# Kernel tuning notes

Measured on AMD Instinct MI355X. Metric: run time of the kernel, lower is better.

The kernel has to match this reference:

```python
import jax, jax.numpy as jnp
import numpy as np

N = 100000
E = 1600000
NEG_SLOPE = 0.2


def _gat_layer(x, src, dst, W, a_src, a_dst, b, heads, out_ch):
    n = x.shape[0]
    h = (x @ W).reshape(n, heads, out_ch)                      # [N,H,C]
    alpha_src = (h * a_src).sum(-1)                            # [N,H]
    alpha_dst = (h * a_dst).sum(-1)                            # [N,H]
    e = jax.nn.leaky_relu(alpha_src[src] + alpha_dst[dst], NEG_SLOPE)  # [E,H]
    # segment softmax over incoming edges of each destination node
    m = jax.ops.segment_max(e, dst, num_segments=n)            # [N,H]
    ex = jnp.exp(e - m[dst])
    denom = jax.ops.segment_sum(ex, dst, num_segments=n)       # [N,H]
    alpha = ex / (denom[dst] + 1e-16)                          # [E,H]
    msg = h[src] * alpha[:, :, None]                           # [E,H,C]
    out = jax.ops.segment_sum(msg, dst, num_segments=n)        # [N,H,C]
    return out.reshape(n, heads * out_ch) + b


def setup_inputs() -> dict:
    key = jax.random.key(0)
    ks = jax.random.split(key, 10)
    glorot = lambda k, shape: jax.random.normal(k, shape, jnp.float32) * np.sqrt(2.0 / (shape[0] + shape[-1]))
    x = jax.random.normal(ks[0], (N, 5), jnp.float32)
    edge_index = jax.random.randint(ks[1], (2, E), 0, N, jnp.int64)
    return {
        "x": x,
        "edge_index": edge_index,
        "W1": glorot(ks[2], (5, 64)),
        "a_src1": glorot(ks[3], (8, 8)),
        "a_dst1": glorot(ks[4], (8, 8)),
        "b1": jnp.zeros((64,), jnp.float32),
        "W2": glorot(ks[5], (64, 2)),
        "a_src2": glorot(ks[6], (1, 2)),
        "a_dst2": glorot(ks[7], (1, 2)),
        "b2": jnp.zeros((2,), jnp.float32),
    }


def reference(x, edge_index, W1, a_src1, a_dst1, b1, W2, a_src2, a_dst2, b2):
    n = x.shape[0]
    loop = jnp.arange(n, dtype=edge_index.dtype)
    src = jnp.concatenate([edge_index[0], loop])   # PyG GATConv adds self-loops
    dst = jnp.concatenate([edge_index[1], loop])
    # dropout layers are no-ops in eval mode
    h = jax.nn.elu(_gat_layer(x, src, dst, W1, a_src1, a_dst1, b1, heads=8, out_ch=8))
    out = _gat_layer(h, src, dst, W2, a_src2, a_dst2, b2, heads=1, out_ch=2)
    return jax.nn.log_softmax(out, axis=1)
```

## Files before the change

### kernel.cpp

```cpp
#include <hip/hip_runtime.h>
#include <hip/hip_fp16.h>
#include <math.h>
#include <stdint.h>

#define N_NODES 100000
#define N_EDGES 1600000
#define N_TOT   (N_EDGES + N_NODES)
#define NEG_SLOPE 0.2f
#define LOG2E 1.44269504088896340736f

#define CB     128
#define CBBITS 7
#define NCB    ((N_NODES + CB - 1) / CB)
#define TP     2048
#define NPB    ((N_EDGES + TP - 1) / TP)
#define WINB   2560
#define NB_NODE1 ((N_NODES * 8 + 511) / 512)

typedef int nt_int4 __attribute__((ext_vector_type(4)));

__global__ void __launch_bounds__(512) k_np(
        const int* __restrict__ src, const int* __restrict__ dst,
        int* __restrict__ ofsT, unsigned* __restrict__ pairs,
        const float* __restrict__ x, const float* __restrict__ W1,
        const float* __restrict__ a_src1, const float* __restrict__ a_dst1,
        __half* __restrict__ xh, __half* __restrict__ as1h,
        float* __restrict__ ad1) {
    __shared__ int lcnt[1024];
    __shared__ int sm[512];
    __shared__ unsigned stage[TP];
    int t = threadIdx.x;

    if (blockIdx.x >= NPB) {
        int gid  = (blockIdx.x - NPB) * 512 + t;
        int n    = gid >> 3;
        int head = gid & 7;
        if (n >= N_NODES) return;

        float xv[5];
#pragma unroll
        for (int k = 0; k < 5; ++k) xv[k] = x[n * 5 + k];

        float as = 0.f, ad = 0.f;
#pragma unroll
        for (int j = 0; j < 8; ++j) {
            int c = head * 8 + j;
            float acc = 0.f;
#pragma unroll
            for (int k = 0; k < 5; ++k) acc += xv[k] * W1[k * 64 + c];
            as += acc * a_src1[c];
            ad += acc * a_dst1[c];
        }
        as1h[n * 8 + head] = __float2half(as * LOG2E);
        ad1[n * 8 + head] = ad * LOG2E;

        if (head == 0) {
            __half2 p0 = __halves2half2(__float2half(xv[0]), __float2half(xv[1]));
            __half2 p1 = __halves2half2(__float2half(xv[2]), __float2half(xv[3]));
            __half2 p2 = __halves2half2(__float2half(xv[4]), __float2half(0.f));
            __half2 p3 = __halves2half2(__float2half(0.f), __float2half(0.f));
            __half2* xp = (__half2*)&xh[(size_t)n * 8];
            xp[0] = p0; xp[1] = p1; xp[2] = p2; xp[3] = p3;
        }
        return;
    }

    int blk = blockIdx.x;
    int base = blk * TP + t * 4;
    bool act = base < N_EDGES;
    int nE = min(TP, N_EDGES - blk * TP);

    lcnt[t] = 0; lcnt[t + 512] = 0;
    __syncthreads();

    nt_int4 s4, d4;
    if (act) {
        s4 = __builtin_nontemporal_load((const nt_int4*)(src + base));
        d4 = __builtin_nontemporal_load((const nt_int4*)(dst + base));
#pragma unroll
        for (int j = 0; j < 4; ++j) atomicAdd(&lcnt[d4[j] >> CBBITS], 1);
    }
    __syncthreads();

    int b0 = lcnt[t * 2], b1 = lcnt[t * 2 + 1];
    int local = b0 + b1;
    sm[t] = local;
    __syncthreads();
    for (int off = 1; off < 512; off <<= 1) {
        int u = (t >= off) ? sm[t - off] : 0;
        __syncthreads();
        sm[t] += u;
        __syncthreads();
    }
    int run = sm[t] - local;
    lcnt[t * 2] = run; lcnt[t * 2 + 1] = run + b0;
    if (t * 2     <= NCB) ofsT[(size_t)(t * 2)     * NPB + blk] = run;
    if (t * 2 + 1 <= NCB) ofsT[(size_t)(t * 2 + 1) * NPB + blk] = run + b0;
    __syncthreads();

    if (act) {
#pragma unroll
        for (int j = 0; j < 4; ++j) {
            int d = d4[j], s = s4[j];
            int bin = d >> CBBITS;
            int idx = atomicAdd(&lcnt[bin], 1);
            stage[idx] = ((unsigned)(d & (CB - 1)) << 17) | (unsigned)s;
        }
    }
    __syncthreads();
    for (int i = t; i < nE; i += 512)
        pairs[(size_t)blk * TP + i] = stage[i];
}

__global__ void __launch_bounds__(512) k_csr(
        const int* __restrict__ ofsT, const unsigned* __restrict__ pairs,
        int* __restrict__ rbeg, int* __restrict__ rend, int* __restrict__ ssrc) {
    __shared__ unsigned stIn[WINB];
    __shared__ int stOut[WINB];
    __shared__ int lcnt[CB], lofs[CB], lcur[CB];
    __shared__ int wsum[2];
    __shared__ int acur;
    int B = blockIdx.x, t = threadIdx.x;
    int nvalid = min(CB, N_NODES - B * CB);
    int obase = B * WINB;

    if (t < CB) {
        lcnt[t] = (t < nvalid) ? 1 : 0;
        lcur[t] = 1;
    }
    if (t == 0) acur = 0;
    __syncthreads();

    for (int blk = t; blk < NPB; blk += 512) {
        int o0 = ofsT[(size_t)B       * NPB + blk];
        int o1 = ofsT[(size_t)(B + 1) * NPB + blk];
        int n = o1 - o0;
        if (n > 0) {
            int p = atomicAdd(&acur, n);
            const unsigned* pp = pairs + (size_t)blk * TP + o0;
            for (int i = 0; i < n; ++i) {
                unsigned r = pp[i];
                stIn[p + i] = r;
                atomicAdd(&lcnt[r >> 17], 1);
            }
        }
    }
    __syncthreads();
    int m = acur;

    int v = (t < CB) ? lcnt[t] : 0;
    int ln = t & 63, wv = t >> 6;
    int sc = v;
#pragma unroll
    for (int off = 1; off < 64; off <<= 1) {
        int u = __shfl_up(sc, off, 64);
        if (ln >= off) sc += u;
    }
    if (ln == 63 && wv < 2) wsum[wv] = sc;
    __syncthreads();
    int wbase = (wv == 1) ? wsum[0] : 0;
    int ex = wbase + sc - v;
    if (t < CB) {
        lofs[t] = ex;
        int gi = B * CB + t;
        if (gi < N_NODES) {
            rbeg[gi] = obase + ex;
            rend[gi] = obase + ex + v;
            stOut[ex] = gi;
        }
    }
    __syncthreads();

    for (int k = t; k < m; k += 512) {
        unsigned p = stIn[k];
        int dl = p >> 17;
        int idx = atomicAdd(&lcur[dl], 1);
        stOut[lofs[dl] + idx] = (int)(p & 0x1FFFF);
    }
    __syncthreads();

    int tot = m + nvalid;
    for (int i = t; i < tot; i += 512) ssrc[obase + i] = stOut[i];
}

__global__ void __launch_bounds__(256) k_gather1(
        const int* __restrict__ rbeg, const int* __restrict__ rend,
        const int* __restrict__ ssrc, const float4* __restrict__ xh4,
        const __half* __restrict__ as1h, const float* __restrict__ ad1,
        float* __restrict__ xsbuf) {
    int gtid = blockIdx.x * blockDim.x + threadIdx.x;
    int d      = gtid >> 5;
    int lane32 = threadIdx.x & 31;
    if (d >= N_NODES) return;
    int e = lane32 >> 3;
    int h = lane32 & 7;

    int beg = rbeg[d], end = rend[d];
    float adv = ad1[d * 8 + h];
    float c0 = 0.f, c1 = 0.f, c2 = 0.f, c3 = 0.f, c4 = 0.f, den = 0.f;

    for (int k = beg; k < end; k += 8) {
        int kA = k + e, kB = k + 4 + e;
        bool vA = kA < end, vB = kB < end;
        int sA = ssrc[vA ? kA : beg];
        int sB = ssrc[vB ? kB : beg];
        float eA = __half2float(as1h[sA * 8 + h]);
        float eB = __half2float(as1h[sB * 8 + h]);
        float4 xA = xh4[sA];
        float4 xB = xh4[sB];
        float tA = eA + adv; tA = fmaxf(tA, NEG_SLOPE * tA);
        float tB = eB + adv; tB = fmaxf(tB, NEG_SLOPE * tB);
        float wA = vA ? __builtin_amdgcn_exp2f(tA) : 0.f;
        float wB = vB ? __builtin_amdgcn_exp2f(tB) : 0.f;
        float2 A01 = __half22float2(*(__half2*)&xA.x);
        float2 A23 = __half22float2(*(__half2*)&xA.y);
        float2 A4_ = __half22float2(*(__half2*)&xA.z);
        float2 B01 = __half22float2(*(__half2*)&xB.x);
        float2 B23 = __half22float2(*(__half2*)&xB.y);
        float2 B4_ = __half22float2(*(__half2*)&xB.z);
        c0 += wA * A01.x + wB * B01.x;
        c1 += wA * A01.y + wB * B01.y;
        c2 += wA * A23.x + wB * B23.x;
        c3 += wA * A23.y + wB * B23.y;
        c4 += wA * A4_.x + wB * B4_.x;
        den += wA + wB;
    }

#define REDH(x) x += __shfl_xor(x, 8, 64); x += __shfl_xor(x, 16, 64);
    REDH(c0) REDH(c1) REDH(c2) REDH(c3) REDH(c4) REDH(den)
#undef REDH

    if (e == 0) {
        float inv = 1.f / den;
        float* xp = xsbuf + ((size_t)d * 8 + h) * 6;
        *(float2*)(xp + 0) = make_float2(c0 * inv, c1 * inv);
        *(float2*)(xp + 2) = make_float2(c2 * inv, c3 * inv);
        *(float2*)(xp + 4) = make_float2(c4 * inv, 0.f);
    }
}

__global__ void __launch_bounds__(256) k_rec(
        const float* __restrict__ xsbuf, const float* __restrict__ b1,
        const float* __restrict__ W1, const float* __restrict__ W2,
        const float* __restrict__ a_src2, const float* __restrict__ a_dst2,
        float4* __restrict__ rec) {
    int gtid = blockIdx.x * blockDim.x + threadIdx.x;
    int d = gtid >> 3;
    int h = gtid & 7;
    if (d >= N_NODES) return;

    const float* xp = xsbuf + ((size_t)d * 8 + h) * 6;
    float2 p0 = *(const float2*)(xp + 0);
    float2 p1 = *(const float2*)(xp + 2);
    float2 p2 = *(const float2*)(xp + 4);
    float xs[5] = { p0.x, p0.y, p1.x, p1.y, p2.x };

    float4 hA = ((const float4*)b1)[2 * h];
    float4 hB = ((const float4*)b1)[2 * h + 1];
#pragma unroll
    for (int c = 0; c < 5; ++c) {
        float xc = xs[c];
        float4 wA = *(const float4*)(W1 + c * 64 + 8 * h);
        float4 wB = *(const float4*)(W1 + c * 64 + 8 * h + 4);
        hA.x += xc * wA.x; hA.y += xc * wA.y; hA.z += xc * wA.z; hA.w += xc * wA.w;
        hB.x += xc * wB.x; hB.y += xc * wB.y; hB.z += xc * wB.z; hB.w += xc * wB.w;
    }
    float v0 = hA.x, v1 = hA.y, v2 = hA.z, v3 = hA.w;
    float v4 = hB.x, v5 = hB.y, v6 = hB.z, v7 = hB.w;
    v0 = (v0 > 0.f) ? v0 : (__expf(v0) - 1.f);
    v1 = (v1 > 0.f) ? v1 : (__expf(v1) - 1.f);
    v2 = (v2 > 0.f) ? v2 : (__expf(v2) - 1.f);
    v3 = (v3 > 0.f) ? v3 : (__expf(v3) - 1.f);
    v4 = (v4 > 0.f) ? v4 : (__expf(v4) - 1.f);
    v5 = (v5 > 0.f) ? v5 : (__expf(v5) - 1.f);
    v6 = (v6 > 0.f) ? v6 : (__expf(v6) - 1.f);
    v7 = (v7 > 0.f) ? v7 : (__expf(v7) - 1.f);

    const float4* w4 = (const float4*)(W2 + h * 16);
    float4 wq0 = w4[0], wq1 = w4[1], wq2 = w4[2], wq3 = w4[3];
    float h20 = v0 * wq0.x + v1 * wq0.z + v2 * wq1.x + v3 * wq1.z
              + v4 * wq2.x + v5 * wq2.z + v6 * wq3.x + v7 * wq3.z;
    float h21 = v0 * wq0.y + v1 * wq0.w + v2 * wq1.y + v3 * wq1.w
              + v4 * wq2.y + v5 * wq2.w + v6 * wq3.y + v7 * wq3.w;
    h20 += __shfl_xor(h20, 1, 64); h20 += __shfl_xor(h20, 2, 64); h20 += __shfl_xor(h20, 4, 64);
    h21 += __shfl_xor(h21, 1, 64); h21 += __shfl_xor(h21, 2, 64); h21 += __shfl_xor(h21, 4, 64);

    if (h == 0) {
        float as2v = h20 * a_src2[0] + h21 * a_src2[1];
        float ad2v = h20 * a_dst2[0] + h21 * a_dst2[1];
        rec[d] = make_float4(h20, h21, as2v, ad2v);
    }
}

__global__ void k_gather2(const int* __restrict__ rbeg, const int* __restrict__ rend,
                          const int* __restrict__ ssrc, const float4* __restrict__ rec,
                          const float* __restrict__ b2, float* __restrict__ out) {
    int gtid = blockIdx.x * blockDim.x + threadIdx.x;
    int d    = gtid >> 4;
    int lane = gtid & 15;
    if (d >= N_NODES) return;

    int beg = rbeg[d], end = rend[d];
    float adv = rec[d].w;
    float n0 = 0.f, n1 = 0.f, den = 0.f;
    int k = beg + lane;
    for (; k + 16 < end; k += 32) {
        int s0 = ssrc[k], s1 = ssrc[k + 16];
        float4 r0 = rec[s0];
        float4 r1 = rec[s1];
        float t0 = r0.z + adv; t0 = fmaxf(t0, NEG_SLOPE * t0);
        float t1 = r1.z + adv; t1 = fmaxf(t1, NEG_SLOPE * t1);
        float w0 = __expf(t0), w1 = __expf(t1);
        n0 += w0 * r0.x + w1 * r1.x;
        n1 += w0 * r0.y + w1 * r1.y;
        den += w0 + w1;
    }
    if (k < end) {
        int s = ssrc[k];
        float4 r = rec[s];
        float t = r.z + adv; t = fmaxf(t, NEG_SLOPE * t);
        float w = __expf(t);
        n0 += w * r.x; n1 += w * r.y; den += w;
    }
#pragma unroll
    for (int off = 8; off; off >>= 1) {
        n0  += __shfl_xor(n0,  off, 16);
        n1  += __shfl_xor(n1,  off, 16);
        den += __shfl_xor(den, off, 16);
    }
    if (lane == 0) {
        float o0 = n0 / den + b2[0];
        float o1 = n1 / den + b2[1];
        float m  = fmaxf(o0, o1);
        float lse = m + __logf(__expf(o0 - m) + __expf(o1 - m));
        out[d * 2 + 0] = o0 - lse;
        out[d * 2 + 1] = o1 - lse;
    }
}

extern "C" void kernel_launch(void* const* d_in, const int* in_sizes, int n_in,
                              void* d_out, int out_size, void* d_ws, size_t ws_size,
                              hipStream_t stream) {
    const float* x      = (const float*)d_in[0];
    const int*   ei     = (const int*)d_in[1];
    const float* W1     = (const float*)d_in[2];
    const float* a_src1 = (const float*)d_in[3];
    const float* a_dst1 = (const float*)d_in[4];
    const float* b1     = (const float*)d_in[5];
    const float* W2     = (const float*)d_in[6];
    const float* a_src2 = (const float*)d_in[7];
    const float* a_dst2 = (const float*)d_in[8];
    const float* b2     = (const float*)d_in[9];
    float* out = (float*)d_out;

    const int* src = ei;
    const int* dst = ei + N_EDGES;

    int* rbeg   = (int*)d_ws;
    int* rend   = rbeg + N_NODES;
    int* ssrc   = rend + N_NODES;
    uintptr_t pp = ((uintptr_t)(ssrc + (size_t)NCB * WINB) + 255) & ~(uintptr_t)255;
    float4*   rec  = (float4*)pp;
    float*    ad1  = (float*)(rec + N_NODES);
    __half*   as1h = (__half*)(ad1 + (size_t)N_NODES * 8);
    __half*   xh   = as1h + (size_t)N_NODES * 8;
    uintptr_t rg = ((uintptr_t)(xh + (size_t)N_NODES * 8) + 255) & ~(uintptr_t)255;
    int*      ofsT  = (int*)rg;
    unsigned* pairs = (unsigned*)(ofsT + (size_t)(NCB + 1) * NPB);
    float*    xsbuf = (float*)rg;

    k_np<<<NPB + NB_NODE1, 512, 0, stream>>>(src, dst, ofsT, pairs,
                                             x, W1, a_src1, a_dst1,
                                             xh, as1h, ad1);
    k_csr<<<NCB, 512, 0, stream>>>(ofsT, pairs, rbeg, rend, ssrc);
    k_gather1<<<(N_NODES * 32 + 255) / 256, 256, 0, stream>>>(rbeg, rend, ssrc,
                                                              (const float4*)xh,
                                                              as1h, ad1, xsbuf);
    k_rec<<<(N_NODES * 8 + 255) / 256, 256, 0, stream>>>(xsbuf, b1, W1, W2,
                                                         a_src2, a_dst2, rec);
    k_gather2<<<(N_NODES * 16 + 255) / 256, 256, 0, stream>>>(rbeg, rend, ssrc,
                                                              rec, b2, out);
}
```

Baseline: 162.1 us.

## Use wave-shuffle scan, SoA xsbuf layout, and 8-lane gather2 with exp2

The block-wide prefix sum in the partition kernel becomes a wave-level shuffle scan plus a small cross-wave step, replacing many barrier rounds. The per-node aggregated features move from an interleaved 6-float layout to a structure-of-arrays layout for coalesced writes and reads. The second-layer gather now uses 8 lanes per node instead of 16, with predicated loads and a hardware exp2 on logits prescaled by log2(e), and writes output as a float2. Fewer lanes per node may reduce parallelism for high-degree nodes but cut idle lanes on an average degree of about 17.

```diff
diff --git a/kernel.cpp b/kernel.cpp
--- a/kernel.cpp
+++ b/kernel.cpp
@@ -16,6 +16,7 @@
 #define NPB    ((N_EDGES + TP - 1) / TP)
 #define WINB   2560
 #define NB_NODE1 ((N_NODES * 8 + 511) / 512)
+#define N8     ((size_t)N_NODES * 8)
 
 typedef int nt_int4 __attribute__((ext_vector_type(4)));
 
@@ -27,8 +28,8 @@
         __half* __restrict__ xh, __half* __restrict__ as1h,
         float* __restrict__ ad1) {
     __shared__ int lcnt[1024];
-    __shared__ int sm[512];
     __shared__ unsigned stage[TP];
+    __shared__ int wred[8];
     int t = threadIdx.x;
 
     if (blockIdx.x >= NPB) {
@@ -84,15 +85,26 @@
 
     int b0 = lcnt[t * 2], b1 = lcnt[t * 2 + 1];
     int local = b0 + b1;
-    sm[t] = local;
-    __syncthreads();
-    for (int off = 1; off < 512; off <<= 1) {
-        int u = (t >= off) ? sm[t - off] : 0;
-        __syncthreads();
-        sm[t] += u;
-        __syncthreads();
-    }
-    int run = sm[t] - local;
+    int ln = t & 63, w = t >> 6;
+    int sc = local;
+#pragma unroll
+    for (int off = 1; off < 64; off <<= 1) {
+        int u = __shfl_up(sc, off, 64);
+        if (ln >= off) sc += u;
+    }
+    if (ln == 63) wred[w] = sc;
+    __syncthreads();
+    if (t < 8) {
+        int v = wred[t], s = v;
+#pragma unroll
+        for (int off = 1; off < 8; off <<= 1) {
+            int u = __shfl_up(s, off, 8);
+            if ((t & 7) >= off) s += u;
+        }
+        wred[t] = s - v;
+    }
+    __syncthreads();
+    int run = wred[w] + sc - local;
     lcnt[t * 2] = run; lcnt[t * 2 + 1] = run + b0;
     if (t * 2     <= NCB) ofsT[(size_t)(t * 2)     * NPB + blk] = run;
     if (t * 2 + 1 <= NCB) ofsT[(size_t)(t * 2 + 1) * NPB + blk] = run + b0;
@@ -232,10 +244,12 @@
 
     if (e == 0) {
         float inv = 1.f / den;
-        float* xp = xsbuf + ((size_t)d * 8 + h) * 6;
-        *(float2*)(xp + 0) = make_float2(c0 * inv, c1 * inv);
-        *(float2*)(xp + 2) = make_float2(c2 * inv, c3 * inv);
-        *(float2*)(xp + 4) = make_float2(c4 * inv, 0.f);
+        size_t idx = (size_t)d * 8 + h;
+        xsbuf[idx]          = c0 * inv;
+        xsbuf[N8 + idx]     = c1 * inv;
+        xsbuf[2 * N8 + idx] = c2 * inv;
+        xsbuf[3 * N8 + idx] = c3 * inv;
+        xsbuf[4 * N8 + idx] = c4 * inv;
     }
 }
 
@@ -249,11 +263,9 @@
     int h = gtid & 7;
     if (d >= N_NODES) return;
 
-    const float* xp = xsbuf + ((size_t)d * 8 + h) * 6;
-    float2 p0 = *(const float2*)(xp + 0);
-    float2 p1 = *(const float2*)(xp + 2);
-    float2 p2 = *(const float2*)(xp + 4);
-    float xs[5] = { p0.x, p0.y, p1.x, p1.y, p2.x };
+    size_t idx = (size_t)d * 8 + h;
+    float xs[5] = { xsbuf[idx], xsbuf[N8 + idx], xsbuf[2 * N8 + idx],
+                    xsbuf[3 * N8 + idx], xsbuf[4 * N8 + idx] };
 
     float4 hA = ((const float4*)b1)[2 * h];
     float4 hB = ((const float4*)b1)[2 * h + 1];
@@ -286,55 +298,45 @@
     h21 += __shfl_xor(h21, 1, 64); h21 += __shfl_xor(h21, 2, 64); h21 += __shfl_xor(h21, 4, 64);
 
     if (h == 0) {
-        float as2v = h20 * a_src2[0] + h21 * a_src2[1];
-        float ad2v = h20 * a_dst2[0] + h21 * a_dst2[1];
+        float as2v = (h20 * a_src2[0] + h21 * a_src2[1]) * LOG2E;
+        float ad2v = (h20 * a_dst2[0] + h21 * a_dst2[1]) * LOG2E;
         rec[d] = make_float4(h20, h21, as2v, ad2v);
     }
 }
 
-__global__ void k_gather2(const int* __restrict__ rbeg, const int* __restrict__ rend,
-                          const int* __restrict__ ssrc, const float4* __restrict__ rec,
-                          const float* __restrict__ b2, float* __restrict__ out) {
+__global__ void __launch_bounds__(256) k_gather2(
+        const int* __restrict__ rbeg, const int* __restrict__ rend,
+        const int* __restrict__ ssrc, const float4* __restrict__ rec,
+        const float* __restrict__ b2, float* __restrict__ out) {
     int gtid = blockIdx.x * blockDim.x + threadIdx.x;
-    int d    = gtid >> 4;
-    int lane = gtid & 15;
+    int d    = gtid >> 3;
+    int lane = threadIdx.x & 7;
     if (d >= N_NODES) return;
 
     int beg = rbeg[d], end = rend[d];
     float adv = rec[d].w;
     float n0 = 0.f, n1 = 0.f, den = 0.f;
-    int k = beg + lane;
-    for (; k + 16 < end; k += 32) {
-        int s0 = ssrc[k], s1 = ssrc[k + 16];
-        float4 r0 = rec[s0];
-        float4 r1 = rec[s1];
-        float t0 = r0.z + adv; t0 = fmaxf(t0, NEG_SLOPE * t0);
-        float t1 = r1.z + adv; t1 = fmaxf(t1, NEG_SLOPE * t1);
-        float w0 = __expf(t0), w1 = __expf(t1);
-        n0 += w0 * r0.x + w1 * r1.x;
-        n1 += w0 * r0.y + w1 * r1.y;
-        den += w0 + w1;
-    }
-    if (k < end) {
-        int s = ssrc[k];
+    for (int k = beg; k < end; k += 8) {
+        int ki = k + lane;
+        bool v = ki < end;
+        int s = ssrc[v ? ki : beg];
         float4 r = rec[s];
         float t = r.z + adv; t = fmaxf(t, NEG_SLOPE * t);
-        float w = __expf(t);
+        float w = v ? __builtin_amdgcn_exp2f(t) : 0.f;
         n0 += w * r.x; n1 += w * r.y; den += w;
     }
 #pragma unroll
-    for (int off = 8; off; off >>= 1) {
-        n0  += __shfl_xor(n0,  off, 16);
-        n1  += __shfl_xor(n1,  off, 16);
-        den += __shfl_xor(den, off, 16);
+    for (int off = 1; off < 8; off <<= 1) {
+        n0  += __shfl_xor(n0,  off, 8);
+        n1  += __shfl_xor(n1,  off, 8);
+        den += __shfl_xor(den, off, 8);
     }
     if (lane == 0) {
         float o0 = n0 / den + b2[0];
         float o1 = n1 / den + b2[1];
         float m  = fmaxf(o0, o1);
         float lse = m + __logf(__expf(o0 - m) + __expf(o1 - m));
-        out[d * 2 + 0] = o0 - lse;
-        out[d * 2 + 1] = o1 - lse;
+        *(float2*)(out + (size_t)d * 2) = make_float2(o0 - lse, o1 - lse);
     }
 }
 
@@ -378,6 +380,6 @@
                                                               as1h, ad1, xsbuf);
     k_rec<<<(N_NODES * 8 + 255) / 256, 256, 0, stream>>>(xsbuf, b1, W1, W2,
                                                          a_src2, a_dst2, rec);
-    k_gather2<<<(N_NODES * 16 + 255) / 256, 256, 0, stream>>>(rbeg, rend, ssrc,
-                                                              rec, b2, out);
-}
+    k_gather2<<<(N_NODES * 8 + 255) / 256, 256, 0, stream>>>(rbeg, rend, ssrc,
+                                                             rec, b2, out);
+}
```

Result: no change. 162.9 us (+0.6%).
